# Kernel optimization log

Measured on AMD Instinct MI355X. Metric: run time of the kernel, lower is better.

The kernel has to match this reference:

```python
import jax, jax.numpy as jnp
import numpy as np
from jax import lax

VOCAB = 32000
D = 256      # d_model
N = 16       # n_neurons
NL = 6       # n_layers
DS = 16      # d_state
DC = 4       # d_conv
DI = 512     # d_inner = expand * d_model
DTR = 16     # dt_rank = ceil(D/16)
NH = 4       # attention heads
HD = D // NH
B, L = 1, 128


def setup_inputs() -> dict:
    key = jax.random.key(0)
    ks = list(jax.random.split(key, 32))
    it = iter(ks)

    def rn(shape, scale):
        return jax.random.normal(next(it), shape, jnp.float32) * scale

    p = {}
    p["x"] = jax.random.randint(next(it), (B, L), 0, VOCAB, dtype=jnp.int32)
    p["embedding"] = rn((VOCAB, D), 0.02)
    p["norm1_w"] = jnp.ones((NL, D)); p["norm1_b"] = jnp.zeros((NL, D))
    p["norm2_w"] = jnp.ones((NL, D)); p["norm2_b"] = jnp.zeros((NL, D))
    # Mamba params (stacked over layers)
    p["in_proj_w"] = rn((NL, 2 * DI, D), D ** -0.5)
    p["conv_w"] = rn((NL, DI, DC), DC ** -0.5)
    p["conv_b"] = jnp.zeros((NL, DI))
    p["x_proj_w"] = rn((NL, DTR + 2 * DS, DI), DI ** -0.5)
    p["dt_proj_w"] = rn((NL, DI, DTR), DTR ** -0.5)
    dt0 = jax.random.uniform(next(it), (NL, DI), jnp.float32, 1e-3, 1e-1)
    p["dt_proj_b"] = jnp.log(jnp.expm1(dt0))  # inverse softplus init
    p["A_log"] = jnp.log(jnp.tile(jnp.arange(1.0, DS + 1.0, dtype=jnp.float32), (NL, DI, 1)))
    p["skip_D"] = jnp.ones((NL, DI))
    p["out_proj_w"] = rn((NL, D, DI), DI ** -0.5)
    # cross-neuron MHA params
    p["attn_in_w"] = rn((NL, 3 * D, D), D ** -0.5)
    p["attn_in_b"] = jnp.zeros((NL, 3 * D))
    p["attn_out_w"] = rn((NL, D, D), D ** -0.5)
    p["attn_out_b"] = jnp.zeros((NL, D))
    p["norm_f_w"] = jnp.ones((D,)); p["norm_f_b"] = jnp.zeros((D,))
    p["head_b"] = jnp.zeros((VOCAB,))
    return p


def _ln(x, w, b):
    m = x.mean(-1, keepdims=True)
    v = ((x - m) ** 2).mean(-1, keepdims=True)
    return (x - m) * lax.rsqrt(v + 1e-5) * w + b


def _mamba(x, ipw, cw, cb, xpw, dpw, dpb, alog, dskip, opw):
    # x: (BN, L, D)
    BN, Ls, _ = x.shape
    xz = x @ ipw.T                       # (BN, L, 2*DI)
    u, z = xz[..., :DI], xz[..., DI:]
    # depthwise causal conv1d, kernel DC, left-pad DC-1
    uc = lax.conv_general_dilated(
        u.swapaxes(1, 2), cw[:, None, :], (1,), [(DC - 1, 0)],
        dimension_numbers=("NCH", "OIH", "NCH"), feature_group_count=DI)
    u = jax.nn.silu(uc + cb[None, :, None]).swapaxes(1, 2)  # (BN, L, DI)
    xdbl = u @ xpw.T                     # (BN, L, DTR+2*DS)
    dt = jax.nn.softplus(xdbl[..., :DTR] @ dpw.T + dpb)     # (BN, L, DI)
    Bm = xdbl[..., DTR:DTR + DS]
    Cm = xdbl[..., DTR + DS:]
    A = -jnp.exp(alog)                   # (DI, DS)

    def step(h, ins):
        dt_t, b_t, c_t, u_t = ins        # (BN,DI) (BN,DS) (BN,DS) (BN,DI)
        h = jnp.exp(dt_t[..., None] * A) * h + (dt_t * u_t)[..., None] * b_t[:, None, :]
        return h, jnp.einsum("bds,bs->bd", h, c_t)

    h0 = jnp.zeros((BN, DI, DS), x.dtype)
    _, ys = lax.scan(step, h0, (dt.swapaxes(0, 1), Bm.swapaxes(0, 1),
                                Cm.swapaxes(0, 1), u.swapaxes(0, 1)))
    y = ys.swapaxes(0, 1) + u * dskip
    return (y * jax.nn.silu(z)) @ opw.T


def _mha(x, iw, ib, ow, ob):
    # x: (B*L, N, D); self-attention across neurons
    Bq, S, _ = x.shape
    qkv = x @ iw.T + ib
    q, k, v = jnp.split(qkv, 3, axis=-1)
    q = q.reshape(Bq, S, NH, HD); k = k.reshape(Bq, S, NH, HD); v = v.reshape(Bq, S, NH, HD)
    att = jax.nn.softmax(jnp.einsum("bqhd,bkhd->bhqk", q, k) / np.float32(np.sqrt(HD)), axis=-1)
    o = jnp.einsum("bhqk,bkhd->bqhd", att, v).reshape(Bq, S, D)
    return o @ ow.T + ob


def reference(x, embedding, norm1_w, norm1_b, norm2_w, norm2_b, in_proj_w, conv_w,
              conv_b, x_proj_w, dt_proj_w, dt_proj_b, A_log, skip_D, out_proj_w,
              attn_in_w, attn_in_b, attn_out_w, attn_out_b, norm_f_w, norm_f_b, head_b):
    Bb, Ll = x.shape
    h = embedding[x]                                             # (B, L, D)
    h = jnp.broadcast_to(h[:, None], (Bb, N, Ll, D)).reshape(Bb * N, Ll, D)
    for i in range(NL):
        h = h + _mamba(_ln(h, norm1_w[i], norm1_b[i]), in_proj_w[i], conv_w[i],
                       conv_b[i], x_proj_w[i], dt_proj_w[i], dt_proj_b[i],
                       A_log[i], skip_D[i], out_proj_w[i])
        xc = _ln(h, norm2_w[i], norm2_b[i]).reshape(Bb, N, Ll, D)
        xc = xc.transpose(0, 2, 1, 3).reshape(Bb * Ll, N, D)
        co = _mha(xc, attn_in_w[i], attn_in_b[i], attn_out_w[i], attn_out_b[i])
        h = h + co.reshape(Bb, Ll, N, D).transpose(0, 2, 1, 3).reshape(Bb * N, Ll, D)
    h = h.reshape(Bb, N, Ll, D).mean(axis=1)                     # avg over neurons
    return _ln(h, norm_f_w, norm_f_b) @ embedding.T + head_b     # tied head
```

## Files before the change

kernel.cpp:

```cpp
#include <hip/hip_runtime.h>

constexpr int SEQ    = 128;
constexpr int NVOCAB = 32000;

constexpr size_t O_HA = 0;
constexpr size_t O_HB = O_HA + (size_t)SEQ*256;
constexpr size_t O_U  = O_HB + (size_t)SEQ*256;
constexpr size_t O_DT = O_U  + (size_t)SEQ*512;
constexpr size_t O_ZS = O_DT + (size_t)SEQ*512;
constexpr size_t O_BC = O_ZS + (size_t)SEQ*512;
constexpr size_t O_YG = O_BC + (size_t)SEQ*32;
constexpr size_t O_AH = O_YG + (size_t)SEQ*512;
constexpr size_t O_WC = O_AH + (size_t)SEQ*256;
constexpr size_t O_BB = O_WC + (size_t)6*256*256;

__device__ __forceinline__ float wsum(float p) {
    #pragma unroll
    for (int m = 1; m < 64; m <<= 1) p += __shfl_xor(p, m);
    return p;
}
__device__ __forceinline__ float dot4(float4 a, float4 b) {
    return a.x*b.x + a.y*b.y + a.z*b.z + a.w*b.w;
}

__global__ __launch_bounds__(256) void combo_kernel(
    const float* __restrict__ aiw, const float* __restrict__ aib,
    const float* __restrict__ aow, const float* __restrict__ aob,
    float* __restrict__ wc, float* __restrict__ bc)
{
    __shared__ float sA[32*68];
    __shared__ float sB[32*68];
    const int l  = blockIdx.x >> 4;
    const int t  = blockIdx.x & 15;
    const int r0 = (t >> 2) * 64;
    const int n0 = (t & 3) * 64;
    const int tid = threadIdx.x;

    const float* av = aiw + (size_t)l*768*256 + (size_t)512*256;
    const float* ab = aib + l*768 + 512;
    const float* ow = aow + (size_t)l*256*256;
    const float* ob = aob + l*256;

    const int ar = tid & 63, ah = (tid >> 6) * 8;
    const int bk = tid >> 3, bn = (tid & 7) * 8;
    const float* Ap = ow + (size_t)(r0 + ar)*256 + ah;
    const float* Bp = av + (size_t)bk*256 + n0 + bn;

    const int rg = tid >> 4, cg = tid & 15;

    float4 ra0 = *(const float4*)(Ap);
    float4 ra1 = *(const float4*)(Ap + 4);
    float4 rb0 = *(const float4*)(Bp);
    float4 rb1 = *(const float4*)(Bp + 4);

    float acc[4][4] = {};

    for (int kc = 0; kc < 256; kc += 32) {
        if (kc) __syncthreads();
        sA[(ah+0)*68+ar]=ra0.x; sA[(ah+1)*68+ar]=ra0.y; sA[(ah+2)*68+ar]=ra0.z; sA[(ah+3)*68+ar]=ra0.w;
        sA[(ah+4)*68+ar]=ra1.x; sA[(ah+5)*68+ar]=ra1.y; sA[(ah+6)*68+ar]=ra1.z; sA[(ah+7)*68+ar]=ra1.w;
        *(float4*)&sB[bk*68+bn]   = rb0;
        *(float4*)&sB[bk*68+bn+4] = rb1;
        __syncthreads();
        if (kc + 32 < 256) {
            ra0 = *(const float4*)(Ap + kc + 32);
            ra1 = *(const float4*)(Ap + kc + 36);
            rb0 = *(const float4*)(Bp + (size_t)(kc + 32)*256);
            rb1 = *(const float4*)(Bp + (size_t)(kc + 32)*256 + 4);
        }
        #pragma unroll
        for (int k = 0; k < 32; ++k) {
            float4 a = *(const float4*)&sA[k*68 + rg*4];
            float4 b = *(const float4*)&sB[k*68 + cg*4];
            acc[0][0] += a.x*b.x; acc[0][1] += a.x*b.y; acc[0][2] += a.x*b.z; acc[0][3] += a.x*b.w;
            acc[1][0] += a.y*b.x; acc[1][1] += a.y*b.y; acc[1][2] += a.y*b.z; acc[1][3] += a.y*b.w;
            acc[2][0] += a.z*b.x; acc[2][1] += a.z*b.y; acc[2][2] += a.z*b.z; acc[2][3] += a.z*b.w;
            acc[3][0] += a.w*b.x; acc[3][1] += a.w*b.y; acc[3][2] += a.w*b.z; acc[3][3] += a.w*b.w;
        }
    }

    float* wout = wc + (size_t)l*256*256;
    #pragma unroll
    for (int i = 0; i < 4; ++i) {
        int row = r0 + rg*4 + i;
        float4 o; o.x = acc[i][0]; o.y = acc[i][1]; o.z = acc[i][2]; o.w = acc[i][3];
        *(float4*)&wout[(size_t)row*256 + n0 + cg*4] = o;
    }

    if (n0 == 0 && tid < 64) {
        int c = r0 + tid;
        float b = ob[c];
        for (int j0 = 0; j0 < 256; j0 += 4) {
            float4 a4 = *(const float4*)&ow[(size_t)c*256 + j0];
            float4 b4 = *(const float4*)&ab[j0];
            b += dot4(a4, b4);
        }
        bc[l*256 + c] = b;
    }
}

template<int MR, int KK, int S>
__device__ __forceinline__ void gemm3(
    const float* __restrict__ Wg, const float* __restrict__ A, int AS,
    float* __restrict__ dest, int DS,
    const float* __restrict__ addsrc, int ASS, const float* __restrict__ bias)
{
    constexpr int NST = KK / (4 * S);
    const int tid = threadIdx.x;
    const int tq  = tid & (S - 1);
    const int c0  = (tid / S) * 2;
    const float* Wp0 = Wg + (size_t)c0*KK + tq*4;
    const float* Wp1 = Wp0 + KK;

    float acc0[MR], acc1[MR];
    #pragma unroll
    for (int r = 0; r < MR; ++r) { acc0[r] = 0.f; acc1[r] = 0.f; }

    float4 wa0 = *(const float4*)(Wp0);
    float4 wa1 = *(const float4*)(Wp1);
    float4 wb0 = *(const float4*)(Wp0 + 4*S);
    float4 wb1 = *(const float4*)(Wp1 + 4*S);

    #pragma unroll 1
    for (int st = 0; st < NST; st += 2) {
        float4 na0, na1, nb0, nb1;
        const bool pa = (st + 2 < NST);
        const bool pb = (st + 3 < NST);
        if (pa) { na0 = *(const float4*)(Wp0 + (st+2)*4*S);
                  na1 = *(const float4*)(Wp1 + (st+2)*4*S); }
        if (pb) { nb0 = *(const float4*)(Wp0 + (st+3)*4*S);
                  nb1 = *(const float4*)(Wp1 + (st+3)*4*S); }
        const int k0 = st*4*S + tq*4;
        #pragma unroll
        for (int r = 0; r < MR; ++r) {
            float4 a = *(const float4*)&A[r*AS + k0];
            acc0[r] += dot4(a, wa0);
            acc1[r] += dot4(a, wa1);
        }
        const int k1 = k0 + 4*S;
        #pragma unroll
        for (int r = 0; r < MR; ++r) {
            float4 a = *(const float4*)&A[r*AS + k1];
            acc0[r] += dot4(a, wb0);
            acc1[r] += dot4(a, wb1);
        }
        if (pa) { wa0 = na0; wa1 = na1; }
        if (pb) { wb0 = nb0; wb1 = nb1; }
    }
    #pragma unroll
    for (int m = 1; m < S; m <<= 1) {
        #pragma unroll
        for (int r = 0; r < MR; ++r) {
            acc0[r] += __shfl_xor(acc0[r], m);
            acc1[r] += __shfl_xor(acc1[r], m);
        }
    }
    if (tq == 0) {
        #pragma unroll
        for (int r = 0; r < MR; ++r) {
            float ox = acc0[r], oy = acc1[r];
            if (bias) { ox += bias[c0]; oy += bias[c0+1]; }
            if (addsrc) {
                float2 s = *(const float2*)&addsrc[r*ASS + c0];
                ox += s.x; oy += s.y;
            }
            float2 o; o.x = ox; o.y = oy;
            *(float2*)&dest[r*DS + c0] = o;
        }
    }
}

__device__ __forceinline__ void ln_row(const float* __restrict__ src, float* __restrict__ dst,
                                       const float* __restrict__ w, const float* __restrict__ b)
{
    int lane = threadIdx.x & 63;
    float4 x = *(const float4*)&src[lane*4];
    float sm = wsum(x.x + x.y + x.z + x.w);
    float mean = sm * (1.0f/256.0f);
    float d0 = x.x-mean, d1 = x.y-mean, d2 = x.z-mean, d3 = x.w-mean;
    float var = wsum(d0*d0 + d1*d1 + d2*d2 + d3*d3) * (1.0f/256.0f);
    float rstd = rsqrtf(var + 1e-5f);
    float4 ww = *(const float4*)&w[lane*4];
    float4 bb = *(const float4*)&b[lane*4];
    float4 o;
    o.x = d0*rstd*ww.x + bb.x;
    o.y = d1*rstd*ww.y + bb.y;
    o.z = d2*rstd*ww.z + bb.z;
    o.w = d3*rstd*ww.w + bb.w;
    *(float4*)&dst[lane*4] = o;
}

__global__ __launch_bounds__(1024, 4) void rowk_kernel(
    const int* __restrict__ x, const float* __restrict__ emb,
    const float* __restrict__ n1w_l, const float* __restrict__ n1b_l,
    const float* __restrict__ n2w_l, const float* __restrict__ n2b_l,
    const float* __restrict__ ipw_l, const float* __restrict__ cw_l, const float* __restrict__ cb_l,
    const float* __restrict__ xpw_l, const float* __restrict__ dpw_l, const float* __restrict__ dpb_l,
    const float* __restrict__ opw_l, const float* __restrict__ wc_l, const float* __restrict__ bc_l,
    const float* __restrict__ nfw, const float* __restrict__ nfb,
    const float* __restrict__ hin, float* __restrict__ hout,
    const float* __restrict__ ygv, float* __restrict__ uv, float* __restrict__ dtv,
    float* __restrict__ zsv, float* __restrict__ bcv, float* __restrict__ AH,
    int li)
{
    __shared__ float SM[6336];
    float* hP  = SM;
    float* h1  = SM + 1056;
    float* sLN = SM + 2112;
    float* sAX = SM + 3168;
    float* zR  = SM + 5248;
    float* suR = SM + 5760;
    float* sxR = SM + 6272;

    const int r = blockIdx.x;
    const int tid = threadIdx.x;
    const int lane = tid & 63, wv = tid >> 6;
    int rr[4];
    #pragma unroll
    for (int j = 0; j < 4; ++j) { int v = r - 3 + j; rr[j] = v < 0 ? 0 : v; }

    {
        int hr = tid >> 8, hc = tid & 255;
        if (li <= 1) hP[hr*264 + hc] = emb[(size_t)x[rr[hr]]*256 + hc];
        else         hP[hr*264 + hc] = hin[rr[hr]*256 + hc];
    }
    if (li >= 1) {
        int yr = tid >> 9, yc = tid & 511;
        sAX[yr*520 + yc]     = ygv[rr[yr]*512 + yc];
        sAX[(2+yr)*520 + yc] = ygv[rr[2+yr]*512 + yc];
    }
    __syncthreads();

    float* hC = hP;
    if (li >= 1) {
        gemm3<4,512,8>(opw_l, sAX, 520, h1, 264, hP, 264, nullptr);
        __syncthreads();
        if (wv < 4) ln_row(h1 + wv*264, sLN + wv*264, n2w_l, n2b_l);
        __syncthreads();
        gemm3<4,256,8>(wc_l, sLN, 264, h1, 264, h1, 264, bc_l);
        __syncthreads();
        hC = h1;
        if (tid < 256) hout[r*256 + tid] = h1[3*264 + tid];
        if (li == 6) {
            if (tid < 256) {
                float v = h1[3*264 + tid];
                float s = wsum(v);
                float q = wsum(v*v);
                if (lane == 0) { sxR[wv] = s; sxR[8 + wv] = q; }
            }
            __syncthreads();
            if (tid < 256) {
                float v = h1[3*264 + tid];
                float mean = (sxR[0]+sxR[1]+sxR[2]+sxR[3]) * (1.0f/256.0f);
                float var  = (sxR[8]+sxR[9]+sxR[10]+sxR[11]) * (1.0f/256.0f) - mean*mean;
                float rstd = rsqrtf(var + 1e-5f);
                AH[r*256 + tid] = (v - mean)*rstd*nfw[tid] + nfb[tid];
            }
            return;
        }
    }

    if (wv < 4) ln_row(hC + wv*264, sLN + wv*264, n1w_l, n1b_l);
    __syncthreads();
    gemm3<4,256,4>(ipw_l,                   sLN,         264, sAX, 520, nullptr, 0, nullptr);
    gemm3<1,256,4>(ipw_l + (size_t)512*256, sLN + 3*264, 264, zR,  512, nullptr, 0, nullptr);
    __syncthreads();

    if (tid < 512) {
        int d = tid;
        float4 c4 = *(const float4*)&cw_l[d*4];
        float acc = cb_l[d];
        if (r >= 3) acc += sAX[d]        * c4.x;
        if (r >= 2) acc += sAX[520 + d]  * c4.y;
        if (r >= 1) acc += sAX[1040 + d] * c4.z;
        acc += sAX[1560 + d] * c4.w;
        float sg = acc / (1.0f + __expf(-acc));
        suR[d] = sg;
        uv[r*512 + d] = sg;
        float z = zR[d];
        zsv[r*512 + d] = z / (1.0f + __expf(-z));
    }
    __syncthreads();

    {
        float4 a0 = *(const float4*)&suR[lane*4];
        float4 a1 = *(const float4*)&suR[256 + lane*4];
        float p[3];
        #pragma unroll
        for (int j = 0; j < 3; ++j) {
            int c = wv*3 + j;
            float4 q0 = *(const float4*)&xpw_l[(size_t)c*512 + lane*4];
            float4 q1 = *(const float4*)&xpw_l[(size_t)c*512 + 256 + lane*4];
            p[j] = dot4(a0, q0) + dot4(a1, q1);
        }
        #pragma unroll
        for (int m = 1; m < 64; m <<= 1) {
            #pragma unroll
            for (int j = 0; j < 3; ++j) p[j] += __shfl_xor(p[j], m);
        }
        if (lane == 0) {
            #pragma unroll
            for (int j = 0; j < 3; ++j) sxR[wv*3 + j] = p[j];
        }
    }
    __syncthreads();
    if (tid >= 16 && tid < 48) bcv[r*32 + tid - 16] = sxR[tid];

    if (tid < 512) {
        int d = tid;
        float4 sx0 = *(const float4*)&sxR[0];
        float4 sx1 = *(const float4*)&sxR[4];
        float4 sx2 = *(const float4*)&sxR[8];
        float4 sx3 = *(const float4*)&sxR[12];
        const float4* dp = (const float4*)&dpw_l[(size_t)d*16];
        float acc = dpb_l[d] + dot4(dp[0], sx0) + dot4(dp[1], sx1)
                             + dot4(dp[2], sx2) + dot4(dp[3], sx3);
        dtv[r*512 + d] = fmaxf(acc, 0.0f) + log1pf(__expf(-fabsf(acc)));
    }
}

__global__ __launch_bounds__(64) void scan_kernel(
    const float* __restrict__ dt, const float* __restrict__ u, const float* __restrict__ zs,
    const float* __restrict__ bcv,
    const float* __restrict__ alog_l, const float* __restrict__ dsk_l,
    float* __restrict__ yg)
{
    __shared__ float sdt[4*132];
    __shared__ float su2[4*132];
    __shared__ float sz2[4*132];
    __shared__ float sB [16*132];
    __shared__ float sC [16*132];
    const int tid = threadIdx.x;
    const int s  = tid & 15;
    const int dl = tid >> 4;
    const int d0 = blockIdx.x * 4;
    const int d  = d0 + dl;

    #pragma unroll
    for (int tt = 0; tt < 2; ++tt) {
        const int t = tid + tt*64;
        float4 q;
        q = *(const float4*)&dt[t*512 + d0];
        sdt[0*132+t]=q.x; sdt[1*132+t]=q.y; sdt[2*132+t]=q.z; sdt[3*132+t]=q.w;
        q = *(const float4*)&u[t*512 + d0];
        su2[0*132+t]=q.x; su2[1*132+t]=q.y; su2[2*132+t]=q.z; su2[3*132+t]=q.w;
        q = *(const float4*)&zs[t*512 + d0];
        sz2[0*132+t]=q.x; sz2[1*132+t]=q.y; sz2[2*132+t]=q.z; sz2[3*132+t]=q.w;
        float4 b0 = *(const float4*)&bcv[t*32 + 0];
        float4 b1 = *(const float4*)&bcv[t*32 + 4];
        float4 b2 = *(const float4*)&bcv[t*32 + 8];
        float4 b3 = *(const float4*)&bcv[t*32 + 12];
        sB[ 0*132+t]=b0.x; sB[ 1*132+t]=b0.y; sB[ 2*132+t]=b0.z; sB[ 3*132+t]=b0.w;
        sB[ 4*132+t]=b1.x; sB[ 5*132+t]=b1.y; sB[ 6*132+t]=b1.z; sB[ 7*132+t]=b1.w;
        sB[ 8*132+t]=b2.x; sB[ 9*132+t]=b2.y; sB[10*132+t]=b2.z; sB[11*132+t]=b2.w;
        sB[12*132+t]=b3.x; sB[13*132+t]=b3.y; sB[14*132+t]=b3.z; sB[15*132+t]=b3.w;
        float4 c0 = *(const float4*)&bcv[t*32 + 16];
        float4 c1 = *(const float4*)&bcv[t*32 + 20];
        float4 c2 = *(const float4*)&bcv[t*32 + 24];
        float4 c3 = *(const float4*)&bcv[t*32 + 28];
        sC[ 0*132+t]=c0.x; sC[ 1*132+t]=c0.y; sC[ 2*132+t]=c0.z; sC[ 3*132+t]=c0.w;
        sC[ 4*132+t]=c1.x; sC[ 5*132+t]=c1.y; sC[ 6*132+t]=c1.z; sC[ 7*132+t]=c1.w;
        sC[ 8*132+t]=c2.x; sC[ 9*132+t]=c2.y; sC[10*132+t]=c2.z; sC[11*132+t]=c2.w;
        sC[12*132+t]=c3.x; sC[13*132+t]=c3.y; sC[14*132+t]=c3.z; sC[15*132+t]=c3.w;
    }
    __syncthreads();

    const float a_ds = -__expf(alog_l[d*16 + s]);
    const float dskv = dsk_l[d];
    float hst = 0.0f;
    #pragma unroll 8
    for (int t = 0; t < SEQ; ++t) {
        float dtvv = sdt[dl*132 + t];
        float uvv  = su2[dl*132 + t];
        hst = __expf(dtvv * a_ds) * hst + dtvv * uvv * sB[s*132 + t];
        float p = hst * sC[s*132 + t];
        p += __shfl_xor(p, 1);
        p += __shfl_xor(p, 2);
        p += __shfl_xor(p, 4);
        p += __shfl_xor(p, 8);
        if (s == 0) yg[t*512 + d] = (p + uvv * dskv) * sz2[dl*132 + t];
    }
}

__global__ __launch_bounds__(256) void head_kernel(
    const float* __restrict__ AH, const float* __restrict__ emb,
    const float* __restrict__ hb, float* __restrict__ out)
{
    __shared__ float sA[32*132];
    __shared__ float sW[32*68];
    const int tid = threadIdx.x;
    const int c0  = blockIdx.x * 64;
    const int ar = tid >> 1;
    const int ak = (tid & 1) * 16;
    const int wc = tid & 63;
    const int wk = (tid >> 6) * 8;
    const int rg = tid >> 4;
    const int cg = tid & 15;

    const float* Ap = AH  + (size_t)ar*256 + ak;
    const float* Wp = emb + (size_t)(c0 + wc)*256 + wk;

    float4 ra0 = *(const float4*)(Ap + 0);
    float4 ra1 = *(const float4*)(Ap + 4);
    float4 ra2 = *(const float4*)(Ap + 8);
    float4 ra3 = *(const float4*)(Ap + 12);
    float4 rw0 = *(const float4*)(Wp + 0);
    float4 rw1 = *(const float4*)(Wp + 4);

    float acc[8][4] = {};

    for (int kc = 0; kc < 256; kc += 32) {
        if (kc) __syncthreads();
        sA[(ak+ 0)*132+ar]=ra0.x; sA[(ak+ 1)*132+ar]=ra0.y; sA[(ak+ 2)*132+ar]=ra0.z; sA[(ak+ 3)*132+ar]=ra0.w;
        sA[(ak+ 4)*132+ar]=ra1.x; sA[(ak+ 5)*132+ar]=ra1.y; sA[(ak+ 6)*132+ar]=ra1.z; sA[(ak+ 7)*132+ar]=ra1.w;
        sA[(ak+ 8)*132+ar]=ra2.x; sA[(ak+ 9)*132+ar]=ra2.y; sA[(ak+10)*132+ar]=ra2.z; sA[(ak+11)*132+ar]=ra2.w;
        sA[(ak+12)*132+ar]=ra3.x; sA[(ak+13)*132+ar]=ra3.y; sA[(ak+14)*132+ar]=ra3.z; sA[(ak+15)*132+ar]=ra3.w;
        sW[(wk+0)*68+wc]=rw0.x; sW[(wk+1)*68+wc]=rw0.y; sW[(wk+2)*68+wc]=rw0.z; sW[(wk+3)*68+wc]=rw0.w;
        sW[(wk+4)*68+wc]=rw1.x; sW[(wk+5)*68+wc]=rw1.y; sW[(wk+6)*68+wc]=rw1.z; sW[(wk+7)*68+wc]=rw1.w;
        __syncthreads();
        if (kc + 32 < 256) {
            ra0 = *(const float4*)(Ap + kc + 32);
            ra1 = *(const float4*)(Ap + kc + 36);
            ra2 = *(const float4*)(Ap + kc + 40);
            ra3 = *(const float4*)(Ap + kc + 44);
            rw0 = *(const float4*)(Wp + kc + 32);
            rw1 = *(const float4*)(Wp + kc + 36);
        }
        #pragma unroll
        for (int k = 0; k < 32; ++k) {
            float4 a0 = *(const float4*)&sA[k*132 + rg*8];
            float4 a1 = *(const float4*)&sA[k*132 + rg*8 + 4];
            float4 b  = *(const float4*)&sW[k*68  + cg*4];
            float av[8] = {a0.x,a0.y,a0.z,a0.w, a1.x,a1.y,a1.z,a1.w};
            #pragma unroll
            for (int i = 0; i < 8; ++i) {
                acc[i][0] += av[i]*b.x;
                acc[i][1] += av[i]*b.y;
                acc[i][2] += av[i]*b.z;
                acc[i][3] += av[i]*b.w;
            }
        }
    }

    const int c = c0 + cg*4;
    float4 h4 = *(const float4*)&hb[c];
    #pragma unroll
    for (int i = 0; i < 8; ++i) {
        int r = rg*8 + i;
        float4 o;
        o.x = acc[i][0] + h4.x;
        o.y = acc[i][1] + h4.y;
        o.z = acc[i][2] + h4.z;
        o.w = acc[i][3] + h4.w;
        *(float4*)&out[(size_t)r*NVOCAB + c] = o;
    }
}

extern "C" void kernel_launch(void* const* d_in, const int* in_sizes, int n_in,
                              void* d_out, int out_size, void* d_ws, size_t ws_size,
                              hipStream_t stream)
{
    const int*   xin = (const int*)d_in[0];
    const float* emb = (const float*)d_in[1];
    const float* n1w = (const float*)d_in[2];
    const float* n1b = (const float*)d_in[3];
    const float* n2w = (const float*)d_in[4];
    const float* n2b = (const float*)d_in[5];
    const float* ipw = (const float*)d_in[6];
    const float* cw  = (const float*)d_in[7];
    const float* cb  = (const float*)d_in[8];
    const float* xpw = (const float*)d_in[9];
    const float* dpw = (const float*)d_in[10];
    const float* dpb = (const float*)d_in[11];
    const float* alog= (const float*)d_in[12];
    const float* dsk = (const float*)d_in[13];
    const float* opw = (const float*)d_in[14];
    const float* aiw = (const float*)d_in[15];
    const float* aib = (const float*)d_in[16];
    const float* aow = (const float*)d_in[17];
    const float* aob = (const float*)d_in[18];
    const float* nfw = (const float*)d_in[19];
    const float* nfb = (const float*)d_in[20];
    const float* hb  = (const float*)d_in[21];
    float* ws  = (float*)d_ws;
    float* out = (float*)d_out;

    combo_kernel<<<96, 256, 0, stream>>>(aiw, aib, aow, aob, ws + O_WC, ws + O_BB);

    for (int i = 0; i <= 6; ++i) {
        int ka = i <= 5 ? i : 5;
        int kc = i >= 1 ? i - 1 : 0;
        const float* hin  = (i % 2 == 0) ? ws + O_HA : ws + O_HB;
        float*       hout = (i % 2 == 0) ? ws + O_HB : ws + O_HA;
        rowk_kernel<<<128, 1024, 0, stream>>>(
            xin, emb,
            n1w + ka*256, n1b + ka*256,
            n2w + kc*256, n2b + kc*256,
            ipw + (size_t)ka*1024*256, cw + (size_t)ka*512*4, cb + ka*512,
            xpw + (size_t)ka*48*512, dpw + (size_t)ka*512*16, dpb + ka*512,
            opw + (size_t)kc*256*512,
            ws + O_WC + (size_t)kc*256*256, ws + O_BB + kc*256,
            nfw, nfb,
            hin, hout,
            ws + O_YG, ws + O_U, ws + O_DT, ws + O_ZS, ws + O_BC, ws + O_AH,
            i);
        if (i <= 5)
            scan_kernel<<<128, 64, 0, stream>>>(
                ws + O_DT, ws + O_U, ws + O_ZS, ws + O_BC,
                alog + (size_t)i*512*16, dsk + i*512, ws + O_YG);
    }
    head_kernel<<<NVOCAB/64, 256, 0, stream>>>(ws + O_AH, emb, hb, out);
}
```

Measured before the change: 550.9 us.

## Rewrite head GEMM as register-tiled direct-load kernel and widen scan blocks

The head GEMM drops its LDS-staged tiling. Each thread now keeps a 16-row by 4-column register tile and loads A and embedding rows directly from global memory, with even/odd double buffering, over 250 blocks. This removes shared-memory traffic and barriers but leans on L1/L2 for reuse and needs many registers. The scan kernel now handles 8 channels per 128-thread block instead of 4 per 64, halving the block count.

```diff
diff --git a/kernel.cpp b/kernel.cpp
--- a/kernel.cpp
+++ b/kernel.cpp
@@ -319,33 +319,38 @@
     }
 }
 
-__global__ __launch_bounds__(64) void scan_kernel(
+__global__ __launch_bounds__(128) void scan_kernel(
     const float* __restrict__ dt, const float* __restrict__ u, const float* __restrict__ zs,
     const float* __restrict__ bcv,
     const float* __restrict__ alog_l, const float* __restrict__ dsk_l,
     float* __restrict__ yg)
 {
-    __shared__ float sdt[4*132];
-    __shared__ float su2[4*132];
-    __shared__ float sz2[4*132];
+    __shared__ float sdt[8*132];
+    __shared__ float su2[8*132];
+    __shared__ float sz2[8*132];
     __shared__ float sB [16*132];
     __shared__ float sC [16*132];
     const int tid = threadIdx.x;
     const int s  = tid & 15;
     const int dl = tid >> 4;
-    const int d0 = blockIdx.x * 4;
+    const int d0 = blockIdx.x * 8;
     const int d  = d0 + dl;
 
-    #pragma unroll
-    for (int tt = 0; tt < 2; ++tt) {
-        const int t = tid + tt*64;
-        float4 q;
-        q = *(const float4*)&dt[t*512 + d0];
-        sdt[0*132+t]=q.x; sdt[1*132+t]=q.y; sdt[2*132+t]=q.z; sdt[3*132+t]=q.w;
-        q = *(const float4*)&u[t*512 + d0];
-        su2[0*132+t]=q.x; su2[1*132+t]=q.y; su2[2*132+t]=q.z; su2[3*132+t]=q.w;
-        q = *(const float4*)&zs[t*512 + d0];
-        sz2[0*132+t]=q.x; sz2[1*132+t]=q.y; sz2[2*132+t]=q.z; sz2[3*132+t]=q.w;
+    {
+        const int t = tid;
+        float4 q0, q1;
+        q0 = *(const float4*)&dt[t*512 + d0];
+        q1 = *(const float4*)&dt[t*512 + d0 + 4];
+        sdt[0*132+t]=q0.x; sdt[1*132+t]=q0.y; sdt[2*132+t]=q0.z; sdt[3*132+t]=q0.w;
+        sdt[4*132+t]=q1.x; sdt[5*132+t]=q1.y; sdt[6*132+t]=q1.z; sdt[7*132+t]=q1.w;
+        q0 = *(const float4*)&u[t*512 + d0];
+        q1 = *(const float4*)&u[t*512 + d0 + 4];
+        su2[0*132+t]=q0.x; su2[1*132+t]=q0.y; su2[2*132+t]=q0.z; su2[3*132+t]=q0.w;
+        su2[4*132+t]=q1.x; su2[5*132+t]=q1.y; su2[6*132+t]=q1.z; su2[7*132+t]=q1.w;
+        q0 = *(const float4*)&zs[t*512 + d0];
+        q1 = *(const float4*)&zs[t*512 + d0 + 4];
+        sz2[0*132+t]=q0.x; sz2[1*132+t]=q0.y; sz2[2*132+t]=q0.z; sz2[3*132+t]=q0.w;
+        sz2[4*132+t]=q1.x; sz2[5*132+t]=q1.y; sz2[6*132+t]=q1.z; sz2[7*132+t]=q1.w;
         float4 b0 = *(const float4*)&bcv[t*32 + 0];
         float4 b1 = *(const float4*)&bcv[t*32 + 4];
         float4 b2 = *(const float4*)&bcv[t*32 + 8];
@@ -382,77 +387,69 @@
     }
 }
 
-__global__ __launch_bounds__(256) void head_kernel(
+__global__ __launch_bounds__(256, 1) void head_kernel(
     const float* __restrict__ AH, const float* __restrict__ emb,
     const float* __restrict__ hb, float* __restrict__ out)
 {
-    __shared__ float sA[32*132];
-    __shared__ float sW[32*68];
-    const int tid = threadIdx.x;
-    const int c0  = blockIdx.x * 64;
-    const int ar = tid >> 1;
-    const int ak = (tid & 1) * 16;
-    const int wc = tid & 63;
-    const int wk = (tid >> 6) * 8;
-    const int rg = tid >> 4;
-    const int cg = tid & 15;
-
-    const float* Ap = AH  + (size_t)ar*256 + ak;
-    const float* Wp = emb + (size_t)(c0 + wc)*256 + wk;
-
-    float4 ra0 = *(const float4*)(Ap + 0);
-    float4 ra1 = *(const float4*)(Ap + 4);
-    float4 ra2 = *(const float4*)(Ap + 8);
-    float4 ra3 = *(const float4*)(Ap + 12);
-    float4 rw0 = *(const float4*)(Wp + 0);
-    float4 rw1 = *(const float4*)(Wp + 4);
-
-    float acc[8][4] = {};
-
-    for (int kc = 0; kc < 256; kc += 32) {
-        if (kc) __syncthreads();
-        sA[(ak+ 0)*132+ar]=ra0.x; sA[(ak+ 1)*132+ar]=ra0.y; sA[(ak+ 2)*132+ar]=ra0.z; sA[(ak+ 3)*132+ar]=ra0.w;
-        sA[(ak+ 4)*132+ar]=ra1.x; sA[(ak+ 5)*132+ar]=ra1.y; sA[(ak+ 6)*132+ar]=ra1.z; sA[(ak+ 7)*132+ar]=ra1.w;
-        sA[(ak+ 8)*132+ar]=ra2.x; sA[(ak+ 9)*132+ar]=ra2.y; sA[(ak+10)*132+ar]=ra2.z; sA[(ak+11)*132+ar]=ra2.w;
-        sA[(ak+12)*132+ar]=ra3.x; sA[(ak+13)*132+ar]=ra3.y; sA[(ak+14)*132+ar]=ra3.z; sA[(ak+15)*132+ar]=ra3.w;
-        sW[(wk+0)*68+wc]=rw0.x; sW[(wk+1)*68+wc]=rw0.y; sW[(wk+2)*68+wc]=rw0.z; sW[(wk+3)*68+wc]=rw0.w;
-        sW[(wk+4)*68+wc]=rw1.x; sW[(wk+5)*68+wc]=rw1.y; sW[(wk+6)*68+wc]=rw1.z; sW[(wk+7)*68+wc]=rw1.w;
-        __syncthreads();
-        if (kc + 32 < 256) {
-            ra0 = *(const float4*)(Ap + kc + 32);
-            ra1 = *(const float4*)(Ap + kc + 36);
-            ra2 = *(const float4*)(Ap + kc + 40);
-            ra3 = *(const float4*)(Ap + kc + 44);
-            rw0 = *(const float4*)(Wp + kc + 32);
-            rw1 = *(const float4*)(Wp + kc + 36);
-        }
-        #pragma unroll
-        for (int k = 0; k < 32; ++k) {
-            float4 a0 = *(const float4*)&sA[k*132 + rg*8];
-            float4 a1 = *(const float4*)&sA[k*132 + rg*8 + 4];
-            float4 b  = *(const float4*)&sW[k*68  + cg*4];
-            float av[8] = {a0.x,a0.y,a0.z,a0.w, a1.x,a1.y,a1.z,a1.w};
-            #pragma unroll
-            for (int i = 0; i < 8; ++i) {
-                acc[i][0] += av[i]*b.x;
-                acc[i][1] += av[i]*b.y;
-                acc[i][2] += av[i]*b.z;
-                acc[i][3] += av[i]*b.w;
-            }
-        }
-    }
-
-    const int c = c0 + cg*4;
+    const int tid  = threadIdx.x;
+    const int wv   = tid >> 6;
+    const int lane = tid & 63;
+    const int b  = blockIdx.x;
+    const int cb = b % 125, rb = b / 125;
+    const int r0 = rb*64 + wv*16;
+    const int c  = cb*256 + lane*4;
+
+    const float* Ap = AH  + (size_t)r0*256;
+    const float* Wp = emb + (size_t)c*256;
+
+    float4 aE[16], aO[16], wE[4], wO[4];
+    float acc[16][4];
+    #pragma unroll
+    for (int r = 0; r < 16; ++r) {
+        #pragma unroll
+        for (int j = 0; j < 4; ++j) acc[r][j] = 0.f;
+    }
+
+    #pragma unroll
+    for (int r = 0; r < 16; ++r) aE[r] = *(const float4*)&Ap[r*256];
+    #pragma unroll
+    for (int j = 0; j < 4; ++j)  wE[j] = *(const float4*)&Wp[(size_t)j*256];
+
+    #pragma unroll 1
+    for (int k = 0; k < 256; k += 8) {
+        if (k + 4 < 256) {
+            #pragma unroll
+            for (int r = 0; r < 16; ++r) aO[r] = *(const float4*)&Ap[r*256 + k + 4];
+            #pragma unroll
+            for (int j = 0; j < 4; ++j)  wO[j] = *(const float4*)&Wp[(size_t)j*256 + k + 4];
+        }
+        #pragma unroll
+        for (int r = 0; r < 16; ++r) {
+            #pragma unroll
+            for (int j = 0; j < 4; ++j) acc[r][j] += dot4(aE[r], wE[j]);
+        }
+        if (k + 8 < 256) {
+            #pragma unroll
+            for (int r = 0; r < 16; ++r) aE[r] = *(const float4*)&Ap[r*256 + k + 8];
+            #pragma unroll
+            for (int j = 0; j < 4; ++j)  wE[j] = *(const float4*)&Wp[(size_t)j*256 + k + 8];
+        }
+        #pragma unroll
+        for (int r = 0; r < 16; ++r) {
+            #pragma unroll
+            for (int j = 0; j < 4; ++j) acc[r][j] += dot4(aO[r], wO[j]);
+        }
+    }
+
     float4 h4 = *(const float4*)&hb[c];
     #pragma unroll
-    for (int i = 0; i < 8; ++i) {
-        int r = rg*8 + i;
+    for (int r = 0; r < 16; ++r) {
         float4 o;
-        o.x = acc[i][0] + h4.x;
-        o.y = acc[i][1] + h4.y;
-        o.z = acc[i][2] + h4.z;
-        o.w = acc[i][3] + h4.w;
-        *(float4*)&out[(size_t)r*NVOCAB + c] = o;
+        o.x = acc[r][0] + h4.x;
+        o.y = acc[r][1] + h4.y;
+        o.z = acc[r][2] + h4.z;
+        o.w = acc[r][3] + h4.w;
+        *(float4*)&out[(size_t)(r0 + r)*NVOCAB + c] = o;
     }
 }
 
@@ -505,9 +502,9 @@
             ws + O_YG, ws + O_U, ws + O_DT, ws + O_ZS, ws + O_BC, ws + O_AH,
             i);
         if (i <= 5)
-            scan_kernel<<<128, 64, 0, stream>>>(
+            scan_kernel<<<64, 128, 0, stream>>>(
                 ws + O_DT, ws + O_U, ws + O_ZS, ws + O_BC,
                 alog + (size_t)i*512*16, dsk + i*512, ws + O_YG);
     }
-    head_kernel<<<NVOCAB/64, 256, 0, stream>>>(ws + O_AH, emb, hb, out);
-}
+    head_kernel<<<250, 256, 0, stream>>>(ws + O_AH, emb, hb, out);
+}
```

New measurement: 587.1 us. 6.6% more time.
